# Kernel optimization log

Measured on AMD Instinct MI355X. Metric: run time of the kernel, lower is better.

Reference implementation:

```python
import jax, jax.numpy as jnp
import numpy as np
import math

H = 8          # attention heads
EPS = 1e-5     # LayerNorm eps (PyTorch default)
N = 4          # note_dim (number of modalities / target seq len)


def _ln(x, g, b):
    mu = jnp.mean(x, axis=-1, keepdims=True)
    v = jnp.var(x, axis=-1, keepdims=True)
    return (x - mu) * jax.lax.rsqrt(v + EPS) * g + b


def _mha(q_in, kv_in, Wqkv, bqkv, Wo, bo, mask):
    # q_in: [Sq, B, d], kv_in: [Sk, B, d]; PyTorch MultiheadAttention math (eval, no dropout)
    d = q_in.shape[-1]
    hd = d // H
    Wq, Wk, Wv = jnp.split(Wqkv, 3, axis=0)
    bq, bk, bv = jnp.split(bqkv, 3)
    q = (q_in @ Wq.T + bq).reshape(q_in.shape[0], q_in.shape[1], H, hd)
    k = (kv_in @ Wk.T + bk).reshape(kv_in.shape[0], kv_in.shape[1], H, hd)
    v = (kv_in @ Wv.T + bv).reshape(kv_in.shape[0], kv_in.shape[1], H, hd)
    scores = jnp.einsum('qbhd,kbhd->bhqk', q, k) * (1.0 / math.sqrt(hd))
    scores = jnp.where(mask, jnp.float32(-jnp.inf), scores)
    attn = jax.nn.softmax(scores, axis=-1)
    out = jnp.einsum('bhqk,kbhd->qbhd', attn, v).reshape(q_in.shape)
    return out @ Wo.T + bo


def setup_inputs() -> dict:
    key = jax.random.key(0)
    B, T, d, dff, L = 32, 1024, 512, 2048, 2
    ks = jax.random.split(key, 24)
    f = lambda i, shape: jax.random.normal(ks[i], shape, dtype=jnp.float32)
    p = lambda i, shape: 0.02 * jax.random.normal(ks[i], shape, dtype=jnp.float32)
    return {
        'ctx0': f(0, (B, T, d)), 'ctx1': f(1, (B, T, d)), 'ctx2': f(2, (B, T, d)),
        'h_ctx': f(3, (B, T, d)),
        'h_tgt0': f(4, (B, T, d)), 'h_tgt1': f(5, (B, T, d)),
        'h_tgt2': f(6, (B, T, d)), 'h_tgt3': f(7, (B, T, d)),
        'Wqkv_self': p(8, (L, 3 * d, d)), 'bqkv_self': jnp.zeros((L, 3 * d)),
        'Wo_self': p(9, (L, d, d)), 'bo_self': jnp.zeros((L, d)),
        'Wqkv_cross': p(10, (L, 3 * d, d)), 'bqkv_cross': jnp.zeros((L, 3 * d)),
        'Wo_cross': p(11, (L, d, d)), 'bo_cross': jnp.zeros((L, d)),
        'W1': p(12, (L, dff, d)), 'b1': jnp.zeros((L, dff)),
        'W2': p(13, (L, d, dff)), 'b2': jnp.zeros((L, d)),
        'ln_g': jnp.ones((L, 3, d)), 'ln_b': jnp.zeros((L, 3, d)),
    }


def reference(ctx0, ctx1, ctx2, h_ctx, h_tgt0, h_tgt1, h_tgt2, h_tgt3,
              Wqkv_self, bqkv_self, Wo_self, bo_self,
              Wqkv_cross, bqkv_cross, Wo_cross, bo_cross,
              W1, b1, W2, b2, ln_g, ln_b):
    B, T, d = h_ctx.shape
    BS = B * T
    # stack modalities as the (tiny) sequence axis: [N, batch*time, d]
    tgt = jnp.stack([t.reshape(BS, d) for t in (h_tgt0, h_tgt1, h_tgt2, h_tgt3)], 0)
    mem = jnp.stack([t.reshape(BS, d) for t in (h_ctx, ctx0, ctx1, ctx2)], 0)
    mask = ~jnp.tril(jnp.ones((N, N), dtype=bool))  # True = masked (strict upper tri)
    L = W1.shape[0]
    x = tgt
    for l in range(L):  # post-norm (norm_first=False) decoder layer, eval mode
        sa = _mha(x, x, Wqkv_self[l], bqkv_self[l], Wo_self[l], bo_self[l], mask)
        x = _ln(x + sa, ln_g[l, 0], ln_b[l, 0])
        ca = _mha(x, mem, Wqkv_cross[l], bqkv_cross[l], Wo_cross[l], bo_cross[l], mask)
        x = _ln(x + ca, ln_g[l, 1], ln_b[l, 1])
        ff = jax.nn.relu(x @ W1[l].T + b1[l]) @ W2[l].T + b2[l]
        x = _ln(x + ff, ln_g[l, 2], ln_b[l, 2])
    return x.reshape(N, B, T, d)
```

## Files before the change

kernel.cpp:

```cpp
#include <hip/hip_runtime.h>
#include <stdint.h>

#define BST    32768
#define NMOD   4
#define MTOT   (NMOD*BST)
#define DMODEL 512
#define DFF    2048
#define NH     8
#define HDIM   64
#define NLAYER 2
#define LNEPS  1e-5f

using half8 = __attribute__((ext_vector_type(8))) _Float16;
using half4 = __attribute__((ext_vector_type(4))) _Float16;
using f32x4 = __attribute__((ext_vector_type(4))) float;

__global__ __launch_bounds__(256) void k_f32_to_f16(const float* __restrict__ src,
                                                    _Float16* __restrict__ dst, int n4) {
    int i = blockIdx.x * 256 + threadIdx.x;
    if (i >= n4) return;
    float4 v = ((const float4*)src)[i];
    half4 o = { (_Float16)v.x, (_Float16)v.y, (_Float16)v.z, (_Float16)v.w };
    ((half4*)dst)[i] = o;
}

__global__ __launch_bounds__(256) void k_concat4(const float* __restrict__ s0, const float* __restrict__ s1,
                                                 const float* __restrict__ s2, const float* __restrict__ s3,
                                                 _Float16* __restrict__ dst) {
    size_t i = (size_t)blockIdx.x * 256 + threadIdx.x;
    size_t e = i * 4;
    int j = (int)(e >> 24);
    size_t rem = e & ((1u << 24) - 1);
    const float* s = (j == 0) ? s0 : (j == 1) ? s1 : (j == 2) ? s2 : s3;
    float4 v = *(const float4*)(s + rem);
    half4 o = { (_Float16)v.x, (_Float16)v.y, (_Float16)v.z, (_Float16)v.w };
    *(half4*)(dst + e) = o;
}

__global__ __launch_bounds__(256) void k_gemm_nt(const _Float16* __restrict__ A,
                                                 const _Float16* __restrict__ W,
                                                 const float* __restrict__ bias,
                                                 _Float16* __restrict__ C,
                                                 int K, int ldc, int relu) {
    __shared__ alignas(16) _Float16 As[128 * 32];
    __shared__ alignas(16) _Float16 Bs[128 * 32];
    const int tid  = threadIdx.x;
    const int lane = tid & 63;
    const int wv   = tid >> 6;
    const int quad = lane >> 4;
    const int lr   = lane & 15;
    const int wrow = (wv >> 1) * 64;
    const int wcol = (wv & 1) * 64;
    const size_t m0 = (size_t)blockIdx.x * 128;
    const size_t f0 = (size_t)blockIdx.y * 128;

    const int r0 = tid >> 2;
    const int c0 = tid & 3;
    const int r1 = r0 + 64;

    f32x4 acc[4][4] = {};

    const int nk = K >> 5;
    for (int kt = 0; kt < nk; ++kt) {
        const int kof = kt * 32;
        __syncthreads();
        uint4 a0 = *(const uint4*)(A + (m0 + r0) * (size_t)K + kof + c0 * 8);
        uint4 a1 = *(const uint4*)(A + (m0 + r1) * (size_t)K + kof + c0 * 8);
        uint4 b0 = *(const uint4*)(W + (f0 + r0) * (size_t)K + kof + c0 * 8);
        uint4 b1 = *(const uint4*)(W + (f0 + r1) * (size_t)K + kof + c0 * 8);
        *(uint4*)(As + r0 * 32 + c0 * 8) = a0;
        *(uint4*)(As + r1 * 32 + c0 * 8) = a1;
        *(uint4*)(Bs + r0 * 32 + c0 * 8) = b0;
        *(uint4*)(Bs + r1 * 32 + c0 * 8) = b1;
        __syncthreads();

        half8 af[4], bf[4];
#pragma unroll
        for (int mt = 0; mt < 4; ++mt)
            af[mt] = *(const half8*)(As + (wrow + mt * 16 + lr) * 32 + quad * 8);
#pragma unroll
        for (int nt = 0; nt < 4; ++nt)
            bf[nt] = *(const half8*)(Bs + (wcol + nt * 16 + lr) * 32 + quad * 8);
#pragma unroll
        for (int mt = 0; mt < 4; ++mt)
#pragma unroll
            for (int nt = 0; nt < 4; ++nt)
                acc[mt][nt] = __builtin_amdgcn_mfma_f32_16x16x32_f16(af[mt], bf[nt], acc[mt][nt], 0, 0, 0);
    }

#pragma unroll
    for (int mt = 0; mt < 4; ++mt) {
#pragma unroll
        for (int nt = 0; nt < 4; ++nt) {
            int col = (int)f0 + wcol + nt * 16 + lr;
            float bv = bias ? bias[col] : 0.0f;
#pragma unroll
            for (int r = 0; r < 4; ++r) {
                size_t row = m0 + wrow + mt * 16 + quad * 4 + r;
                float v = acc[mt][nt][r] + bv;
                if (relu) v = v > 0.0f ? v : 0.0f;
                C[row * (size_t)ldc + col] = (_Float16)v;
            }
        }
    }
}

__global__ __launch_bounds__(256) void k_attn(const _Float16* __restrict__ Q,
                                              const _Float16* __restrict__ Kp,
                                              const _Float16* __restrict__ Vp,
                                              int ldq, _Float16* __restrict__ O, int ldo) {
    const int bs = blockIdx.x;
    const int tid = threadIdx.x;
    const int w = tid >> 6;
    const int c = tid & 63;
    for (int hh = 0; hh < 2; ++hh) {
        const int h = w + hh * 4;
        float qv[4], kv[4], vv[4];
#pragma unroll
        for (int i = 0; i < 4; ++i) {
            size_t off = ((size_t)(i * BST + bs)) * ldq + h * 64 + c;
            qv[i] = (float)Q[off];
            kv[i] = (float)Kp[off];
            vv[i] = (float)Vp[off];
        }
        float s[4][4];
#pragma unroll
        for (int i = 0; i < 4; ++i)
#pragma unroll
            for (int j = 0; j < 4; ++j) {
                if (j > i) continue;
                float p = qv[i] * kv[j];
#pragma unroll
                for (int off = 32; off >= 1; off >>= 1) p += __shfl_xor(p, off, 64);
                s[i][j] = p * 0.125f;
            }
#pragma unroll
        for (int i = 0; i < 4; ++i) {
            float mx = s[i][0];
            for (int j = 1; j <= i; ++j) mx = fmaxf(mx, s[i][j]);
            float e[4], sum = 0.0f;
            for (int j = 0; j <= i; ++j) { e[j] = __expf(s[i][j] - mx); sum += e[j]; }
            float inv = 1.0f / sum;
            float o = 0.0f;
            for (int j = 0; j <= i; ++j) o += e[j] * inv * vv[j];
            O[((size_t)(i * BST + bs)) * ldo + h * 64 + c] = (_Float16)o;
        }
    }
}

__global__ __launch_bounds__(256) void k_add_ln(const _Float16* __restrict__ X,
                                                const _Float16* __restrict__ Y,
                                                const float* __restrict__ g,
                                                const float* __restrict__ b,
                                                _Float16* __restrict__ out16,
                                                float* __restrict__ out32) {
    const int tid = threadIdx.x;
    const int w = tid >> 6, c = tid & 63;
    const size_t m = (size_t)blockIdx.x * 4 + w;
    const size_t base = m * DMODEL;
    float v[8];
    float sum = 0.0f;
#pragma unroll
    for (int e = 0; e < 8; ++e) {
        int idx = e * 64 + c;
        v[e] = (float)X[base + idx] + (float)Y[base + idx];
        sum += v[e];
    }
#pragma unroll
    for (int off = 32; off >= 1; off >>= 1) sum += __shfl_xor(sum, off, 64);
    const float mu = sum * (1.0f / 512.0f);
    float vs = 0.0f;
#pragma unroll
    for (int e = 0; e < 8; ++e) { float d = v[e] - mu; vs += d * d; }
#pragma unroll
    for (int off = 32; off >= 1; off >>= 1) vs += __shfl_xor(vs, off, 64);
    const float rs = rsqrtf(vs * (1.0f / 512.0f) + LNEPS);
#pragma unroll
    for (int e = 0; e < 8; ++e) {
        int idx = e * 64 + c;
        float o = (v[e] - mu) * rs * g[idx] + b[idx];
        if (out32) out32[base + idx] = o;
        else       out16[base + idx] = (_Float16)o;
    }
}

extern "C" void kernel_launch(void* const* d_in, const int* in_sizes, int n_in,
                              void* d_out, int out_size, void* d_ws, size_t ws_size,
                              hipStream_t stream) {
    const float* ctx0       = (const float*)d_in[0];
    const float* ctx1       = (const float*)d_in[1];
    const float* ctx2       = (const float*)d_in[2];
    const float* h_ctx      = (const float*)d_in[3];
    const float* h_tgt0     = (const float*)d_in[4];
    const float* h_tgt1     = (const float*)d_in[5];
    const float* h_tgt2     = (const float*)d_in[6];
    const float* h_tgt3     = (const float*)d_in[7];
    const float* Wqkv_self  = (const float*)d_in[8];
    const float* bqkv_self  = (const float*)d_in[9];
    const float* Wo_self    = (const float*)d_in[10];
    const float* bo_self    = (const float*)d_in[11];
    const float* Wqkv_cross = (const float*)d_in[12];
    const float* bqkv_cross = (const float*)d_in[13];
    const float* Wo_cross   = (const float*)d_in[14];
    const float* bo_cross   = (const float*)d_in[15];
    const float* W1         = (const float*)d_in[16];
    const float* b1         = (const float*)d_in[17];
    const float* W2         = (const float*)d_in[18];
    const float* b2         = (const float*)d_in[19];
    const float* ln_g       = (const float*)d_in[20];
    const float* ln_b       = (const float*)d_in[21];

    char* wsb = (char*)d_ws;
    size_t off = 0;
    auto carve = [&](size_t bytes) -> void* {
        void* p = wsb + off;
        off += (bytes + 255) & ~(size_t)255;
        return p;
    };
    _Float16* x     = (_Float16*)carve((size_t)MTOT * DMODEL * 2);
    _Float16* memb  = (_Float16*)carve((size_t)MTOT * DMODEL * 2);
    _Float16* big   = (_Float16*)carve((size_t)MTOT * DFF * 2);
    _Float16* projo = (_Float16*)carve((size_t)MTOT * DMODEL * 2);
    _Float16* wqs = (_Float16*)carve((size_t)NLAYER * 3 * DMODEL * DMODEL * 2);
    _Float16* wos = (_Float16*)carve((size_t)NLAYER * DMODEL * DMODEL * 2);
    _Float16* wqc = (_Float16*)carve((size_t)NLAYER * 3 * DMODEL * DMODEL * 2);
    _Float16* woc = (_Float16*)carve((size_t)NLAYER * DMODEL * DMODEL * 2);
    _Float16* w1h = (_Float16*)carve((size_t)NLAYER * DFF * DMODEL * 2);
    _Float16* w2h = (_Float16*)carve((size_t)NLAYER * DMODEL * DFF * 2);
    _Float16* attno = big + (size_t)MTOT * 1536;

    auto conv = [&](const float* s, _Float16* dst, int n) {
        int n4 = n / 4;
        k_f32_to_f16<<<(n4 + 255) / 256, 256, 0, stream>>>(s, dst, n4);
    };
    conv(Wqkv_self,  wqs, NLAYER * 3 * DMODEL * DMODEL);
    conv(Wo_self,    wos, NLAYER * DMODEL * DMODEL);
    conv(Wqkv_cross, wqc, NLAYER * 3 * DMODEL * DMODEL);
    conv(Wo_cross,   woc, NLAYER * DMODEL * DMODEL);
    conv(W1,         w1h, NLAYER * DFF * DMODEL);
    conv(W2,         w2h, NLAYER * DMODEL * DFF);

    const int concat_blocks = (MTOT * DMODEL / 4) / 256;
    k_concat4<<<concat_blocks, 256, 0, stream>>>(h_tgt0, h_tgt1, h_tgt2, h_tgt3, x);
    k_concat4<<<concat_blocks, 256, 0, stream>>>(h_ctx, ctx0, ctx1, ctx2, memb);

    auto gemm = [&](const _Float16* A, const _Float16* Wp, const float* bias, _Float16* Cc,
                    int K, int F, int ldc, int relu) {
        dim3 g(MTOT / 128, F / 128);
        k_gemm_nt<<<g, 256, 0, stream>>>(A, Wp, bias, Cc, K, ldc, relu);
    };

    for (int l = 0; l < NLAYER; ++l) {
        gemm(x, wqs + (size_t)l * 3 * DMODEL * DMODEL, bqkv_self + l * 3 * DMODEL,
             big, DMODEL, 3 * DMODEL, 3 * DMODEL, 0);
        k_attn<<<BST, 256, 0, stream>>>(big, big + 512, big + 1024, 3 * DMODEL, attno, DMODEL);
        gemm(attno, wos + (size_t)l * DMODEL * DMODEL, bo_self + l * DMODEL,
             projo, DMODEL, DMODEL, DMODEL, 0);
        k_add_ln<<<MTOT / 4, 256, 0, stream>>>(x, projo, ln_g + (l * 3 + 0) * DMODEL,
                                               ln_b + (l * 3 + 0) * DMODEL, x, nullptr);
        const _Float16* Wc = wqc + (size_t)l * 3 * DMODEL * DMODEL;
        gemm(x, Wc, bqkv_cross + l * 3 * DMODEL, big, DMODEL, DMODEL, 3 * DMODEL, 0);
        gemm(memb, Wc + (size_t)DMODEL * DMODEL, bqkv_cross + l * 3 * DMODEL + DMODEL,
             big + 512, DMODEL, 2 * DMODEL, 3 * DMODEL, 0);
        k_attn<<<BST, 256, 0, stream>>>(big, big + 512, big + 1024, 3 * DMODEL, attno, DMODEL);
        gemm(attno, woc + (size_t)l * DMODEL * DMODEL, bo_cross + l * DMODEL,
             projo, DMODEL, DMODEL, DMODEL, 0);
        k_add_ln<<<MTOT / 4, 256, 0, stream>>>(x, projo, ln_g + (l * 3 + 1) * DMODEL,
                                               ln_b + (l * 3 + 1) * DMODEL, x, nullptr);
        gemm(x, w1h + (size_t)l * DFF * DMODEL, b1 + l * DFF, big, DMODEL, DFF, DFF, 1);
        gemm(big, w2h + (size_t)l * DMODEL * DFF, b2 + l * DMODEL, projo, DFF, DMODEL, DMODEL, 0);
        const bool last = (l == NLAYER - 1);
        k_add_ln<<<MTOT / 4, 256, 0, stream>>>(x, projo, ln_g + (l * 3 + 2) * DMODEL,
                                               ln_b + (l * 3 + 2) * DMODEL,
                                               last ? nullptr : x, last ? (float*)d_out : nullptr);
    }
    (void)in_sizes; (void)n_in; (void)out_size; (void)ws_size;
}
```

Baseline: 6.221 ms.

## Use direct global-to-LDS loads in GEMM and vectorize attention and LayerNorm

The GEMM tile loads now use global_load_lds to write straight into LDS instead of going through registers. A trailing barrier is added, and the bias loop order is swapped so bias is loaded once per column. The attention kernel now gives each lane two elements of a head, so all 8 heads are handled in one pass with half2 loads and shorter shuffle reductions. The add+LayerNorm kernel uses 16-byte vector loads and stores. The aim is less register traffic and fewer memory instructions, but global_load_lds requires the LDS layout to match lane order exactly, and there is still no double buffering.

```diff
diff --git a/kernel.cpp b/kernel.cpp
--- a/kernel.cpp
+++ b/kernel.cpp
@@ -13,7 +13,12 @@
 
 using half8 = __attribute__((ext_vector_type(8))) _Float16;
 using half4 = __attribute__((ext_vector_type(4))) _Float16;
+using half2v = __attribute__((ext_vector_type(2))) _Float16;
 using f32x4 = __attribute__((ext_vector_type(4))) float;
+
+#define GLOAD_LDS16(g, l)                                                              \
+    __builtin_amdgcn_global_load_lds((const __attribute__((address_space(1))) void*)(g), \
+                                     (__attribute__((address_space(3))) void*)(l), 16, 0, 0)
 
 __global__ __launch_bounds__(256) void k_f32_to_f16(const float* __restrict__ src,
                                                     _Float16* __restrict__ dst, int n4) {
@@ -54,24 +59,28 @@
     const size_t m0 = (size_t)blockIdx.x * 128;
     const size_t f0 = (size_t)blockIdx.y * 128;
 
-    const int r0 = tid >> 2;
-    const int c0 = tid & 3;
-    const int r1 = r0 + 64;
+    const int ch0  = wv * 64 + lane;
+    const int ch1  = ch0 + 256;
+    const int row0 = ch0 >> 2, c80 = (ch0 & 3) * 8;
+    const int row1 = ch1 >> 2, c81 = (ch1 & 3) * 8;
+    _Float16* As0 = As + (size_t)(wv * 64) * 8;
+    _Float16* As1 = As + (size_t)(256 + wv * 64) * 8;
+    _Float16* Bs0 = Bs + (size_t)(wv * 64) * 8;
+    _Float16* Bs1 = Bs + (size_t)(256 + wv * 64) * 8;
+    const _Float16* Arow0 = A + (m0 + row0) * (size_t)K + c80;
+    const _Float16* Arow1 = A + (m0 + row1) * (size_t)K + c81;
+    const _Float16* Brow0 = W + (f0 + row0) * (size_t)K + c80;
+    const _Float16* Brow1 = W + (f0 + row1) * (size_t)K + c81;
 
     f32x4 acc[4][4] = {};
 
     const int nk = K >> 5;
     for (int kt = 0; kt < nk; ++kt) {
-        const int kof = kt * 32;
-        __syncthreads();
-        uint4 a0 = *(const uint4*)(A + (m0 + r0) * (size_t)K + kof + c0 * 8);
-        uint4 a1 = *(const uint4*)(A + (m0 + r1) * (size_t)K + kof + c0 * 8);
-        uint4 b0 = *(const uint4*)(W + (f0 + r0) * (size_t)K + kof + c0 * 8);
-        uint4 b1 = *(const uint4*)(W + (f0 + r1) * (size_t)K + kof + c0 * 8);
-        *(uint4*)(As + r0 * 32 + c0 * 8) = a0;
-        *(uint4*)(As + r1 * 32 + c0 * 8) = a1;
-        *(uint4*)(Bs + r0 * 32 + c0 * 8) = b0;
-        *(uint4*)(Bs + r1 * 32 + c0 * 8) = b1;
+        const int kof = kt << 5;
+        GLOAD_LDS16(Arow0 + kof, As0);
+        GLOAD_LDS16(Arow1 + kof, As1);
+        GLOAD_LDS16(Brow0 + kof, Bs0);
+        GLOAD_LDS16(Brow1 + kof, Bs1);
         __syncthreads();
 
         half8 af[4], bf[4];
@@ -86,14 +95,15 @@
 #pragma unroll
             for (int nt = 0; nt < 4; ++nt)
                 acc[mt][nt] = __builtin_amdgcn_mfma_f32_16x16x32_f16(af[mt], bf[nt], acc[mt][nt], 0, 0, 0);
-    }
-
-#pragma unroll
-    for (int mt = 0; mt < 4; ++mt) {
-#pragma unroll
-        for (int nt = 0; nt < 4; ++nt) {
-            int col = (int)f0 + wcol + nt * 16 + lr;
-            float bv = bias ? bias[col] : 0.0f;
+        __syncthreads();
+    }
+
+#pragma unroll
+    for (int nt = 0; nt < 4; ++nt) {
+        const int col = (int)f0 + wcol + nt * 16 + lr;
+        const float bv = bias ? bias[col] : 0.0f;
+#pragma unroll
+        for (int mt = 0; mt < 4; ++mt) {
 #pragma unroll
             for (int r = 0; r < 4; ++r) {
                 size_t row = m0 + wrow + mt * 16 + quad * 4 + r;
@@ -113,38 +123,41 @@
     const int tid = threadIdx.x;
     const int w = tid >> 6;
     const int c = tid & 63;
-    for (int hh = 0; hh < 2; ++hh) {
-        const int h = w + hh * 4;
-        float qv[4], kv[4], vv[4];
-#pragma unroll
-        for (int i = 0; i < 4; ++i) {
-            size_t off = ((size_t)(i * BST + bs)) * ldq + h * 64 + c;
-            qv[i] = (float)Q[off];
-            kv[i] = (float)Kp[off];
-            vv[i] = (float)Vp[off];
+    const int h = (w << 1) + (c >> 5);
+    const int e = (c & 31) << 1;
+    float qx[4], qy[4], kx[4], ky[4], vx[4], vy[4];
+#pragma unroll
+    for (int i = 0; i < 4; ++i) {
+        size_t off = ((size_t)(i * BST + bs)) * ldq + h * 64 + e;
+        half2v qq = *(const half2v*)(Q + off);
+        half2v kk = *(const half2v*)(Kp + off);
+        half2v vv = *(const half2v*)(Vp + off);
+        qx[i] = (float)qq.x; qy[i] = (float)qq.y;
+        kx[i] = (float)kk.x; ky[i] = (float)kk.y;
+        vx[i] = (float)vv.x; vy[i] = (float)vv.y;
+    }
+    float s[4][4];
+#pragma unroll
+    for (int i = 0; i < 4; ++i)
+#pragma unroll
+        for (int j = 0; j < 4; ++j) {
+            if (j > i) continue;
+            float p = qx[i] * kx[j] + qy[i] * ky[j];
+#pragma unroll
+            for (int off = 16; off >= 1; off >>= 1) p += __shfl_xor(p, off, 64);
+            s[i][j] = p * 0.125f;
         }
-        float s[4][4];
-#pragma unroll
-        for (int i = 0; i < 4; ++i)
-#pragma unroll
-            for (int j = 0; j < 4; ++j) {
-                if (j > i) continue;
-                float p = qv[i] * kv[j];
-#pragma unroll
-                for (int off = 32; off >= 1; off >>= 1) p += __shfl_xor(p, off, 64);
-                s[i][j] = p * 0.125f;
-            }
-#pragma unroll
-        for (int i = 0; i < 4; ++i) {
-            float mx = s[i][0];
-            for (int j = 1; j <= i; ++j) mx = fmaxf(mx, s[i][j]);
-            float e[4], sum = 0.0f;
-            for (int j = 0; j <= i; ++j) { e[j] = __expf(s[i][j] - mx); sum += e[j]; }
-            float inv = 1.0f / sum;
-            float o = 0.0f;
-            for (int j = 0; j <= i; ++j) o += e[j] * inv * vv[j];
-            O[((size_t)(i * BST + bs)) * ldo + h * 64 + c] = (_Float16)o;
-        }
+#pragma unroll
+    for (int i = 0; i < 4; ++i) {
+        float mx = s[i][0];
+        for (int j = 1; j <= i; ++j) mx = fmaxf(mx, s[i][j]);
+        float ee[4], sum = 0.0f;
+        for (int j = 0; j <= i; ++j) { ee[j] = __expf(s[i][j] - mx); sum += ee[j]; }
+        float inv = 1.0f / sum;
+        float ox = 0.0f, oy = 0.0f;
+        for (int j = 0; j <= i; ++j) { ox += ee[j] * vx[j]; oy += ee[j] * vy[j]; }
+        half2v o = { (_Float16)(ox * inv), (_Float16)(oy * inv) };
+        *(half2v*)(O + ((size_t)(i * BST + bs)) * ldo + h * 64 + e) = o;
     }
 }
 
@@ -157,15 +170,13 @@
     const int tid = threadIdx.x;
     const int w = tid >> 6, c = tid & 63;
     const size_t m = (size_t)blockIdx.x * 4 + w;
-    const size_t base = m * DMODEL;
+    const size_t base = m * DMODEL + (size_t)c * 8;
+    half8 xv = *(const half8*)(X + base);
+    half8 yv = *(const half8*)(Y + base);
     float v[8];
     float sum = 0.0f;
 #pragma unroll
-    for (int e = 0; e < 8; ++e) {
-        int idx = e * 64 + c;
-        v[e] = (float)X[base + idx] + (float)Y[base + idx];
-        sum += v[e];
-    }
+    for (int e = 0; e < 8; ++e) { v[e] = (float)xv[e] + (float)yv[e]; sum += v[e]; }
 #pragma unroll
     for (int off = 32; off >= 1; off >>= 1) sum += __shfl_xor(sum, off, 64);
     const float mu = sum * (1.0f / 512.0f);
@@ -175,12 +186,22 @@
 #pragma unroll
     for (int off = 32; off >= 1; off >>= 1) vs += __shfl_xor(vs, off, 64);
     const float rs = rsqrtf(vs * (1.0f / 512.0f) + LNEPS);
-#pragma unroll
-    for (int e = 0; e < 8; ++e) {
-        int idx = e * 64 + c;
-        float o = (v[e] - mu) * rs * g[idx] + b[idx];
-        if (out32) out32[base + idx] = o;
-        else       out16[base + idx] = (_Float16)o;
+    float gv[8], bv[8];
+    *(float4*)(gv)     = *(const float4*)(g + c * 8);
+    *(float4*)(gv + 4) = *(const float4*)(g + c * 8 + 4);
+    *(float4*)(bv)     = *(const float4*)(b + c * 8);
+    *(float4*)(bv + 4) = *(const float4*)(b + c * 8 + 4);
+    if (out32) {
+        float o[8];
+#pragma unroll
+        for (int e = 0; e < 8; ++e) o[e] = (v[e] - mu) * rs * gv[e] + bv[e];
+        *(float4*)(out32 + base)     = *(float4*)(o);
+        *(float4*)(out32 + base + 4) = *(float4*)(o + 4);
+    } else {
+        half8 o;
+#pragma unroll
+        for (int e = 0; e < 8; ++e) o[e] = (_Float16)((v[e] - mu) * rs * gv[e] + bv[e]);
+        *(half8*)(out16 + base) = o;
     }
 }
 
```

Result: faster. 6.056 ms (-2.6%).
